# Performance work log

Measured on AMD Instinct MI355X. Metric: run time of the kernel, lower is better.

## Reference

```python
import jax, jax.numpy as jnp
import numpy as np

E = 1024   # embed_dim
H = 16     # num_heads
D = E // H # head_dim
T = 1024   # tgt_len
S = 1024   # src_len
B = 2      # batch
DELTA = 1.0
SCALE = D ** -0.5


def setup_inputs() -> dict:
    key = jax.random.key(0)
    ks = jax.random.split(key, 16)
    def lin(k, o, i):
        return jax.random.normal(k, (o, i), dtype=jnp.float32) / np.float32(np.sqrt(i))
    return {
        'query': jax.random.normal(ks[0], (T, B, E), dtype=jnp.float32),
        'key_in': jax.random.normal(ks[1], (S, B, E), dtype=jnp.float32),
        'value': jax.random.normal(ks[2], (S, B, E), dtype=jnp.float32),
        'Wq': lin(ks[3], E, E), 'bq': jnp.zeros((E,), jnp.float32),
        'Wk': lin(ks[4], E, E), 'bk': jnp.zeros((E,), jnp.float32),
        'Wv': lin(ks[5], E, E), 'bv': jnp.zeros((E,), jnp.float32),
        'Whq': lin(ks[6], E, E), 'bhq': jnp.zeros((E,), jnp.float32),
        'Whk': lin(ks[7], E, E), 'bhk': jnp.zeros((E,), jnp.float32),
        'Wwp': lin(ks[8], E, E), 'bwp': jnp.zeros((E,), jnp.float32),
        'Wvp': lin(ks[9], 1, E), 'bvp': jnp.zeros((1,), jnp.float32),
        'Wo': lin(ks[10], E, E), 'bo': jnp.zeros((E,), jnp.float32),
    }


def _heads(x, L):
    # (L, B, E) -> (B*H, L, D); E splits as (H, D) so flat index is b*H + h
    return x.reshape(L, B * H, D).transpose(1, 0, 2)


def reference(query, key_in, value, Wq, bq, Wk, bk, Wv, bv, Whq, bhq, Whk, bhk,
              Wwp, bwp, Wvp, bvp, Wo, bo):
    q = (query @ Wq.T + bq) * SCALE
    k = key_in @ Wk.T + bk
    v = value @ Wv.T + bv
    hq = query @ Whq.T + bhq
    hk = key_in @ Whk.T + bhk

    qh, hqh = _heads(q, T), _heads(hq, T)
    kh, hkh, vh = _heads(k, S), _heads(hk, S), _heads(v, S)

    # content attention logits  [B*H, T, S]
    attn = jnp.einsum('btd,bsd->bts', qh, kh)

    # Gaussian center: expected source position from hq/hk alignment
    align = jax.nn.softmax(jnp.einsum('btd,bsd->bts', hqh * SCALE, hkh), axis=-1)
    pos = jnp.arange(S, dtype=attn.dtype)          # index_mask
    mean = align @ pos                              # [B*H, T]

    # Gaussian width: per-query scalar via vp(tanh(wp(query)))
    g = (jnp.tanh(query @ Wwp.T + bwp) @ Wvp.T + bvp)[..., 0]   # (T, B)
    sigma = 1.0 + DELTA * jax.nn.sigmoid(g)                      # (T, B)
    sigma_bh = jnp.broadcast_to(sigma[:, :, None], (T, B, H)).reshape(T, B * H).T

    gauss = -((pos[None, None, :] - mean[:, :, None]) ** 2) / (
        2.0 * sigma_bh[:, :, None] ** 2)

    probs = jax.nn.softmax(attn + gauss, axis=-1)
    out = jnp.einsum('bts,bsd->btd', probs, vh)     # [B*H, T, D]
    out = out.transpose(1, 0, 2).reshape(T, B, E)
    return out @ Wo.T + bo
```

## Files before the change

kernel.cpp:

```cpp
#include <hip/hip_runtime.h>
#include <hip/hip_bf16.h>
#include <hip/hip_fp16.h>

#define T_ 1024
#define S_ 1024
#define B_ 2
#define H_ 16
#define D_ 64
#define E_ 1024
#define M_ (T_*B_)
#define SCALE_ 0.125f
#define LOG2E_ 1.4426950408889634f

typedef __attribute__((ext_vector_type(8))) short short8;
typedef __attribute__((ext_vector_type(8))) _Float16 half8;
typedef __attribute__((ext_vector_type(4))) float f32x4;

#define EXP2 __builtin_amdgcn_exp2f

__device__ __forceinline__ ushort f2bf(float x) {
  unsigned u = __float_as_uint(x);
  unsigned r = (u + 0x7fffu + ((u >> 16) & 1u)) >> 16;
  return (ushort)r;
}
__device__ __forceinline__ float bf2f(ushort h) {
  return __uint_as_float(((unsigned)h) << 16);
}
__device__ __forceinline__ ushort f2h(float x) {
  __half h = __float2half(x);
  return *(ushort*)&h;
}
__device__ __forceinline__ void gld16(const void* g, void* l) {
  __builtin_amdgcn_global_load_lds(
      (const __attribute__((address_space(1))) void*)g,
      (__attribute__((address_space(3))) void*)l, 16, 0, 0);
}
__device__ __forceinline__ unsigned cvtpk_bf16(float a, float b) {
  unsigned u;
  asm("v_cvt_pk_bf16_f32 %0, %1, %2" : "=v"(u) : "v"(a), "v"(b));
  return u;
}

#define SWZ(r, col) ((r)*64 + ((col) ^ (((r)&7)<<3)))

struct CvtDesc { const float* src; ushort* bf; ushort* h16; int n4; };
struct CvtArgs { CvtDesc d[10]; };

__global__ __launch_bounds__(256) void cvt_kernel(CvtArgs a) {
  const CvtDesc d = a.d[blockIdx.y];
  const int stride = gridDim.x * 256;
  for (int i = blockIdx.x*256 + threadIdx.x; i < d.n4; i += stride) {
    float4 v = ((const float4*)d.src)[i];
    float vals[4] = {v.x, v.y, v.z, v.w};
    if (d.bf) {
      ushort h[4];
      #pragma unroll
      for (int j = 0; j < 4; ++j) h[j] = f2bf(vals[j]);
      ((ushort4*)d.bf)[i] = make_ushort4(h[0],h[1],h[2],h[3]);
    }
    if (d.h16) {
      ushort h[4];
      #pragma unroll
      for (int j = 0; j < 4; ++j) h[j] = f2h(vals[j]);
      ((ushort4*)d.h16)[i] = make_ushort4(h[0],h[1],h[2],h[3]);
    }
  }
}

struct SegP { const ushort* A; const ushort* W; const float* bias;
              ushort* outb; float* outf; float scale; int flags; };
struct GemmArgs { SegP s[6]; };

__global__ __launch_bounds__(256) void gemm_mfma(GemmArgs args) {
  __shared__ ushort sA[2][128*64];
  __shared__ ushort sW[2][128*64];
  const SegP sg = args.s[blockIdx.x >> 3];
  const int n0 = (blockIdx.x & 7) * 128;
  const int m0 = blockIdx.y * 128;
  const int tid = threadIdx.x, wv = tid >> 6, lane = tid & 63;
  const int c = lane & 15, g = lane >> 4;
  const int wr = wv >> 1, wc = wv & 1;
  const int lrow = lane >> 3;
  const int scol = ((lane & 7) ^ lrow) * 8;

  size_t aoff[4], woff[4];
  #pragma unroll
  for (int j = 0; j < 4; ++j) {
    int rg = wv + j*4;
    aoff[j] = (size_t)(m0 + rg*8 + lrow)*1024 + scol;
    woff[j] = (size_t)(n0 + rg*8 + lrow)*1024 + scol;
  }

  const bool isfp16 = (sg.flags & 2) != 0;
  f32x4 acc[4][4] = {};
  #pragma unroll
  for (int j = 0; j < 4; ++j) {
    int rg = wv + j*4;
    gld16(sg.A + aoff[j], &sA[0][rg*512]);
    gld16(sg.W + woff[j], &sW[0][rg*512]);
  }
  __syncthreads();

  for (int t = 0; t < 16; ++t) {
    const int cur = t & 1;
    if (t < 15) {
      const int k0 = (t+1)*64;
      #pragma unroll
      for (int j = 0; j < 4; ++j) {
        int rg = wv + j*4;
        gld16(sg.A + aoff[j] + k0, &sA[cur^1][rg*512]);
        gld16(sg.W + woff[j] + k0, &sW[cur^1][rg*512]);
      }
    }
    #pragma unroll
    for (int ks = 0; ks < 2; ++ks) {
      short8 af[4], wf[4];
      #pragma unroll
      for (int mi = 0; mi < 4; ++mi)
        af[mi] = *(const short8*)&sA[cur][SWZ(wr*64 + mi*16 + c, ks*32 + g*8)];
      #pragma unroll
      for (int ni = 0; ni < 4; ++ni)
        wf[ni] = *(const short8*)&sW[cur][SWZ(wc*64 + ni*16 + c, ks*32 + g*8)];
      if (isfp16) {
        #pragma unroll
        for (int mi = 0; mi < 4; ++mi)
          #pragma unroll
          for (int ni = 0; ni < 4; ++ni)
            acc[mi][ni] = __builtin_amdgcn_mfma_f32_16x16x32_f16(
                *(half8*)&af[mi], *(half8*)&wf[ni], acc[mi][ni], 0, 0, 0);
      } else {
        #pragma unroll
        for (int mi = 0; mi < 4; ++mi)
          #pragma unroll
          for (int ni = 0; ni < 4; ++ni)
            acc[mi][ni] = __builtin_amdgcn_mfma_f32_16x16x32_bf16(
                af[mi], wf[ni], acc[mi][ni], 0, 0, 0);
      }
    }
    __syncthreads();
  }

  #pragma unroll
  for (int ni = 0; ni < 4; ++ni) {
    int col = n0 + wc*64 + ni*16 + c;
    float bias = sg.bias[col];
    #pragma unroll
    for (int mi = 0; mi < 4; ++mi) {
      #pragma unroll
      for (int r = 0; r < 4; ++r) {
        int row = m0 + wr*64 + mi*16 + 4*g + r;
        float val = (acc[mi][ni][r] + bias) * sg.scale;
        if (sg.flags & 1) val = tanhf(val);
        if (isfp16)       sg.outb[(size_t)row*1024 + col] = f2h(val);
        else if (sg.outf) sg.outf[(size_t)row*1024 + col] = val;
        else              sg.outb[(size_t)row*1024 + col] = f2bf(val);
      }
    }
  }
}

__global__ __launch_bounds__(64) void vp_sigma(const ushort* __restrict__ wp,
    const float* __restrict__ Wvp, const float* __restrict__ bvp,
    float* __restrict__ sigma) {
  const int m = blockIdx.x;
  const int lane = threadIdx.x;
  float acc = 0.f;
  #pragma unroll
  for (int it = 0; it < 2; ++it) {
    int e = lane*8 + it*512;
    short8 a = *(const short8*)&wp[(size_t)m*E_ + e];
    float4 w0 = *(const float4*)&Wvp[e];
    float4 w1 = *(const float4*)&Wvp[e+4];
    acc += bf2f((ushort)a[0])*w0.x + bf2f((ushort)a[1])*w0.y
         + bf2f((ushort)a[2])*w0.z + bf2f((ushort)a[3])*w0.w
         + bf2f((ushort)a[4])*w1.x + bf2f((ushort)a[5])*w1.y
         + bf2f((ushort)a[6])*w1.z + bf2f((ushort)a[7])*w1.w;
  }
  #pragma unroll
  for (int o = 32; o; o >>= 1) acc += __shfl_xor(acc, o);
  if (lane == 0) {
    float gg = acc + bvp[0];
    sigma[m] = 1.f + 1.f/(1.f + __expf(-gg));
  }
}

__global__ __launch_bounds__(256) void attn_mfma(
    const ushort* __restrict__ q_bf, const ushort* __restrict__ k_bf,
    const ushort* __restrict__ v_bf,
    const ushort* __restrict__ hq_h16, const ushort* __restrict__ hk_h16,
    const float* __restrict__ sigma, ushort* __restrict__ ctx) {
  __shared__ ushort sK[2][64*64];
  __shared__ ushort sV[2][64*64];
  __shared__ ushort sP[4*16*64];

  const int bh = blockIdx.y;
  const int b = bh >> 4, h = bh & 15;
  const int t0 = blockIdx.x * 64;
  const int tid = threadIdx.x;
  const int wv = tid >> 6, lane = tid & 63;
  const int c = lane & 15, g = lane >> 4;
  const int qbase = t0 + wv * 16;
  const size_t rowstr = (size_t)B_ * E_;
  const size_t qoff = ((size_t)(qbase + c) * B_ + b) * E_ + h * 64;

  short8 qf[2];
  half8  hqf[2];
  #pragma unroll
  for (int cs = 0; cs < 2; ++cs) {
    qf[cs]  = *(const short8*)&q_bf[qoff + cs*32 + g*8];
    hqf[cs] = *(const half8*)&hq_h16[qoff + cs*32 + g*8];
  }

  const int str0 = wv*16 + (lane >> 3);
  const int str1 = str0 + 8;
  const int chk0 = ((lane & 7) ^ (str0 & 7)) * 8;
  const int chk1 = ((lane & 7) ^ (str1 & 7)) * 8;
  const int ldsst = (wv*16) * 64;

  float den = 0.f, num = 0.f;
  {
    gld16(hk_h16 + ((size_t)str0 * B_ + b) * E_ + h*64 + chk0, &sK[0][ldsst]);
    gld16(hk_h16 + ((size_t)str1 * B_ + b) * E_ + h*64 + chk1, &sK[0][ldsst + 512]);
    __syncthreads();
    for (int t = 0; t < 16; ++t) {
      const ushort* kb = sK[t & 1];
      if (t < 15) {
        int s0n = (t+1) * 64;
        gld16(hk_h16 + ((size_t)(s0n + str0) * B_ + b) * E_ + h*64 + chk0,
              &sK[(t+1) & 1][ldsst]);
        gld16(hk_h16 + ((size_t)(s0n + str1) * B_ + b) * E_ + h*64 + chk1,
              &sK[(t+1) & 1][ldsst + 512]);
      }
      f32x4 acc[4] = {};
      __builtin_amdgcn_s_setprio(1);
      #pragma unroll
      for (int m = 0; m < 4; ++m)
        #pragma unroll
        for (int cs = 0; cs < 2; ++cs)
          acc[m] = __builtin_amdgcn_mfma_f32_16x16x32_f16(
              *(const half8*)&kb[SWZ(c + 16*m, cs*32 + g*8)], hqf[cs], acc[m], 0,0,0);
      __builtin_amdgcn_s_setprio(0);

      float fs = (float)(t*64 + 4*g);
      #pragma unroll
      for (int m = 0; m < 4; ++m)
        #pragma unroll
        for (int r = 0; r < 4; ++r) {
          float e = EXP2(acc[m][r]);
          den += e;
          num += e * (fs + (float)(16*m + r));
        }
      __syncthreads();
    }
  }
  den += __shfl_xor(den, 16); den += __shfl_xor(den, 32);
  num += __shfl_xor(num, 16); num += __shfl_xor(num, 32);
  const float meanq = num / den;
  const float sg = sigma[(size_t)(qbase + c) * B_ + b];
  const float fct = -LOG2E_ / (2.f * sg * sg);

  f32x4 accO[4] = {};
  float denq = 0.f;
  {
    gld16(k_bf + ((size_t)str0 * B_ + b) * E_ + h*64 + chk0, &sK[0][ldsst]);
    gld16(k_bf + ((size_t)str1 * B_ + b) * E_ + h*64 + chk1, &sK[0][ldsst + 512]);
    {
      int s2 = (tid & 31) * 2, d0 = (tid >> 5) * 8;
      size_t off0 = ((size_t)s2 * B_ + b) * E_ + h * 64 + d0;
      uint4 ra = *(const uint4*)&v_bf[off0];
      uint4 rb = *(const uint4*)&v_bf[off0 + rowstr];
      const ushort* pa = (const ushort*)&ra;
      const ushort* pb = (const ushort*)&rb;
      #pragma unroll
      for (int j = 0; j < 8; ++j)
        *(unsigned*)&sV[0][SWZ(d0 + j, s2)] = (unsigned)pa[j] | ((unsigned)pb[j] << 16);
    }
    __syncthreads();

    const int s2v = (tid & 31) * 2, d0v = (tid >> 5) * 8;
    for (int t = 0; t < 16; ++t) {
      const int cur = t & 1;
      const ushort* kb = sK[cur];
      const ushort* vb = sV[cur];
      uint4 ra, rb;
      if (t < 15) {
        int s0n = (t+1) * 64;
        gld16(k_bf + ((size_t)(s0n + str0) * B_ + b) * E_ + h*64 + chk0,
              &sK[cur^1][ldsst]);
        gld16(k_bf + ((size_t)(s0n + str1) * B_ + b) * E_ + h*64 + chk1,
              &sK[cur^1][ldsst + 512]);
        size_t off0 = ((size_t)(s0n + s2v) * B_ + b) * E_ + h * 64 + d0v;
        ra = *(const uint4*)&v_bf[off0];
        rb = *(const uint4*)&v_bf[off0 + rowstr];
      }

      f32x4 accL[4] = {};
      __builtin_amdgcn_s_setprio(1);
      #pragma unroll
      for (int m = 0; m < 4; ++m)
        #pragma unroll
        for (int cs = 0; cs < 2; ++cs)
          accL[m] = __builtin_amdgcn_mfma_f32_16x16x32_bf16(
              *(const short8*)&kb[SWZ(c + 16*m, cs*32 + g*8)], qf[cs], accL[m], 0,0,0);
      __builtin_amdgcn_s_setprio(0);

      float fs = (float)(t*64 + 4*g);
      float psum = 0.f;
      #pragma unroll
      for (int m = 0; m < 4; ++m) {
        float pr[4];
        #pragma unroll
        for (int r = 0; r < 4; ++r) {
          float dd = fs + (float)(16*m + r) - meanq;
          pr[r] = EXP2(accL[m][r] + fct * dd * dd);
          psum += pr[r];
        }
        uint2 uu;
        uu.x = cvtpk_bf16(pr[0], pr[1]);
        uu.y = cvtpk_bf16(pr[2], pr[3]);
        *(uint2*)&sP[wv*1024 + SWZ(c, 16*m + 4*g)] = uu;
      }
      denq += psum;

      __builtin_amdgcn_s_setprio(1);
      #pragma unroll
      for (int n = 0; n < 4; ++n)
        #pragma unroll
        for (int cs = 0; cs < 2; ++cs)
          accO[n] = __builtin_amdgcn_mfma_f32_16x16x32_bf16(
              *(const short8*)&sP[wv*1024 + SWZ(c, cs*32 + 8*g)],
              *(const short8*)&vb[SWZ(c + 16*n, cs*32 + 8*g)],
              accO[n], 0,0,0);
      __builtin_amdgcn_s_setprio(0);

      if (t < 15) {
        const ushort *pa = (const ushort*)&ra, *pb = (const ushort*)&rb;
        #pragma unroll
        for (int j = 0; j < 8; ++j)
          *(unsigned*)&sV[cur^1][SWZ(d0v + j, s2v)] = (unsigned)pa[j] | ((unsigned)pb[j] << 16);
      }
      __syncthreads();
    }
  }

  denq += __shfl_xor(denq, 16);
  denq += __shfl_xor(denq, 32);
  float dinv[4];
  #pragma unroll
  for (int r = 0; r < 4; ++r) dinv[r] = 1.f / __shfl(denq, 4*g + r);

  #pragma unroll
  for (int r = 0; r < 4; ++r) {
    size_t row = ((size_t)(qbase + 4*g + r) * B_ + b) * E_ + h * 64;
    #pragma unroll
    for (int n = 0; n < 4; ++n)
      ctx[row + 16*n + c] = f2bf(accO[n][r] * dinv[r]);
  }
}

extern "C" void kernel_launch(void* const* d_in, const int* in_sizes, int n_in,
                              void* d_out, int out_size, void* d_ws, size_t ws_size,
                              hipStream_t stream) {
  const float* query  = (const float*)d_in[0];
  const float* key_in = (const float*)d_in[1];
  const float* value  = (const float*)d_in[2];
  const float* Wq  = (const float*)d_in[3];  const float* bq  = (const float*)d_in[4];
  const float* Wk  = (const float*)d_in[5];  const float* bk  = (const float*)d_in[6];
  const float* Wv  = (const float*)d_in[7];  const float* bv  = (const float*)d_in[8];
  const float* Whq = (const float*)d_in[9];  const float* bhq = (const float*)d_in[10];
  const float* Whk = (const float*)d_in[11]; const float* bhk = (const float*)d_in[12];
  const float* Wwp = (const float*)d_in[13]; const float* bwp = (const float*)d_in[14];
  const float* Wvp = (const float*)d_in[15]; const float* bvp = (const float*)d_in[16];
  const float* Wo  = (const float*)d_in[17]; const float* bo  = (const float*)d_in[18];

  const size_t AU = (size_t)M_ * E_;
  const size_t WU = (size_t)E_ * E_;
  char* p = (char*)d_ws;
  float*  sig       = (float*)p;  p += 16384;
  ushort* query_bf  = (ushort*)p; p += AU*2;
  ushort* key_bf    = (ushort*)p; p += AU*2;
  ushort* value_bf  = (ushort*)p; p += AU*2;
  ushort* query_h16 = (ushort*)p; p += AU*2;
  ushort* key_h16   = (ushort*)p; p += AU*2;
  ushort* Whq_h16   = (ushort*)p; p += WU*2;
  ushort* Whk_h16   = (ushort*)p; p += WU*2;
  ushort* Wq_bf     = (ushort*)p; p += WU*2;
  ushort* Wk_bf     = (ushort*)p; p += WU*2;
  ushort* Wv_bf     = (ushort*)p; p += WU*2;
  ushort* Wwp_bf    = (ushort*)p; p += WU*2;
  ushort* Wo_bf     = (ushort*)p; p += WU*2;
  ushort* hq_h16    = (ushort*)p; p += AU*2;
  ushort* hk_h16    = (ushort*)p; p += AU*2;
  ushort* q_bf      = (ushort*)p; p += AU*2;
  ushort* k_bf      = (ushort*)p; p += AU*2;
  ushort* v_out     = (ushort*)p; p += AU*2;
  ushort* wp_bf     = (ushort*)p; p += AU*2;
  ushort* ctx_bf    = query_h16;

  {
    CvtArgs a{};
    a.d[0] = {query,  query_bf, query_h16, (int)(AU/4)};
    a.d[1] = {key_in, key_bf,   key_h16,   (int)(AU/4)};
    a.d[2] = {value,  value_bf, nullptr,   (int)(AU/4)};
    a.d[3] = {Whq,    nullptr,  Whq_h16,   (int)(WU/4)};
    a.d[4] = {Whk,    nullptr,  Whk_h16,   (int)(WU/4)};
    a.d[5] = {Wq,     Wq_bf,    nullptr,   (int)(WU/4)};
    a.d[6] = {Wk,     Wk_bf,    nullptr,   (int)(WU/4)};
    a.d[7] = {Wv,     Wv_bf,    nullptr,   (int)(WU/4)};
    a.d[8] = {Wwp,    Wwp_bf,   nullptr,   (int)(WU/4)};
    a.d[9] = {Wo,     Wo_bf,    nullptr,   (int)(WU/4)};
    cvt_kernel<<<dim3(128, 10), 256, 0, stream>>>(a);
  }
  {
    GemmArgs a{};
    a.s[0] = {query_bf,  Wq_bf,   bq,  q_bf,   nullptr, SCALE_*LOG2E_, 0};
    a.s[1] = {query_bf,  Wwp_bf,  bwp, wp_bf,  nullptr, 1.f,           1};
    a.s[2] = {key_bf,    Wk_bf,   bk,  k_bf,   nullptr, 1.f,           0};
    a.s[3] = {value_bf,  Wv_bf,   bv,  v_out,  nullptr, 1.f,           0};
    a.s[4] = {query_h16, Whq_h16, bhq, hq_h16, nullptr, SCALE_*LOG2E_, 2};
    a.s[5] = {key_h16,   Whk_h16, bhk, hk_h16, nullptr, 1.f,           2};
    gemm_mfma<<<dim3(48, 16), 256, 0, stream>>>(a);
  }
  vp_sigma<<<dim3(M_), dim3(64), 0, stream>>>(wp_bf, Wvp, bvp, sig);
  attn_mfma<<<dim3(T_/64, B_*H_), dim3(256), 0, stream>>>(
      q_bf, k_bf, v_out, hq_h16, hk_h16, sig, ctx_bf);
  {
    GemmArgs a{};
    a.s[0] = {ctx_bf, Wo_bf, bo, nullptr, (float*)d_out, 1.f, 0};
    gemm_mfma<<<dim3(8, 16), 256, 0, stream>>>(a);
  }
}
```

Before: 137.4 us.

## Remap blocks to XCDs for L2 locality and single-buffer GEMM LDS

Grids become 1D, and block ids are remapped so that consecutive blocks landing on the same XCD (round-robin dispatch across the eight XCDs) share the same weight columns or the same attention head, which should improve L2 reuse. The GEMM also drops LDS double buffering in favour of a single buffer with load-then-sync per k-step. That halves LDS use and may raise occupancy, but it removes the overlap of global loads with MFMA work. The single-buffer loop appears to rely on the trailing barrier to avoid overwriting data still being read.

```diff
diff --git a/kernel.cpp b/kernel.cpp
--- a/kernel.cpp
+++ b/kernel.cpp
@@ -72,11 +72,15 @@
 struct GemmArgs { SegP s[6]; };
 
 __global__ __launch_bounds__(256) void gemm_mfma(GemmArgs args) {
-  __shared__ ushort sA[2][128*64];
-  __shared__ ushort sW[2][128*64];
-  const SegP sg = args.s[blockIdx.x >> 3];
-  const int n0 = (blockIdx.x & 7) * 128;
-  const int m0 = blockIdx.y * 128;
+  __shared__ ushort sA[128*64];
+  __shared__ ushort sW[128*64];
+  const int id = blockIdx.x;
+  const int xcd = id & 7, loc = id >> 3;
+  const int x = xcd * (gridDim.x >> 7) + (loc >> 4);
+  const int y = loc & 15;
+  const SegP sg = args.s[x >> 3];
+  const int n0 = (x & 7) * 128;
+  const int m0 = y * 128;
   const int tid = threadIdx.x, wv = tid >> 6, lane = tid & 63;
   const int c = lane & 15, g = lane >> 4;
   const int wr = wv >> 1, wc = wv & 1;
@@ -93,34 +97,24 @@
 
   const bool isfp16 = (sg.flags & 2) != 0;
   f32x4 acc[4][4] = {};
-  #pragma unroll
-  for (int j = 0; j < 4; ++j) {
-    int rg = wv + j*4;
-    gld16(sg.A + aoff[j], &sA[0][rg*512]);
-    gld16(sg.W + woff[j], &sW[0][rg*512]);
-  }
-  __syncthreads();
-
   for (int t = 0; t < 16; ++t) {
-    const int cur = t & 1;
-    if (t < 15) {
-      const int k0 = (t+1)*64;
-      #pragma unroll
-      for (int j = 0; j < 4; ++j) {
-        int rg = wv + j*4;
-        gld16(sg.A + aoff[j] + k0, &sA[cur^1][rg*512]);
-        gld16(sg.W + woff[j] + k0, &sW[cur^1][rg*512]);
-      }
-    }
+    const int k0 = t*64;
+    #pragma unroll
+    for (int j = 0; j < 4; ++j) {
+      int rg = wv + j*4;
+      gld16(sg.A + aoff[j] + k0, &sA[rg*512]);
+      gld16(sg.W + woff[j] + k0, &sW[rg*512]);
+    }
+    __syncthreads();
     #pragma unroll
     for (int ks = 0; ks < 2; ++ks) {
       short8 af[4], wf[4];
       #pragma unroll
       for (int mi = 0; mi < 4; ++mi)
-        af[mi] = *(const short8*)&sA[cur][SWZ(wr*64 + mi*16 + c, ks*32 + g*8)];
+        af[mi] = *(const short8*)&sA[SWZ(wr*64 + mi*16 + c, ks*32 + g*8)];
       #pragma unroll
       for (int ni = 0; ni < 4; ++ni)
-        wf[ni] = *(const short8*)&sW[cur][SWZ(wc*64 + ni*16 + c, ks*32 + g*8)];
+        wf[ni] = *(const short8*)&sW[SWZ(wc*64 + ni*16 + c, ks*32 + g*8)];
       if (isfp16) {
         #pragma unroll
         for (int mi = 0; mi < 4; ++mi)
@@ -193,9 +187,11 @@
   __shared__ ushort sV[2][64*64];
   __shared__ ushort sP[4*16*64];
 
-  const int bh = blockIdx.y;
+  const int id = blockIdx.x;
+  const int loc = id >> 3;
+  const int bh = (id & 7) * 4 + (loc >> 4);
   const int b = bh >> 4, h = bh & 15;
-  const int t0 = blockIdx.x * 64;
+  const int t0 = (loc & 15) * 64;
   const int tid = threadIdx.x;
   const int wv = tid >> 6, lane = tid & 63;
   const int c = lane & 15, g = lane >> 4;
@@ -419,14 +415,14 @@
     a.s[3] = {value_bf,  Wv_bf,   bv,  v_out,  nullptr, 1.f,           0};
     a.s[4] = {query_h16, Whq_h16, bhq, hq_h16, nullptr, SCALE_*LOG2E_, 2};
     a.s[5] = {key_h16,   Whk_h16, bhk, hk_h16, nullptr, 1.f,           2};
-    gemm_mfma<<<dim3(48, 16), 256, 0, stream>>>(a);
+    gemm_mfma<<<dim3(768), 256, 0, stream>>>(a);
   }
   vp_sigma<<<dim3(M_), dim3(64), 0, stream>>>(wp_bf, Wvp, bvp, sig);
-  attn_mfma<<<dim3(T_/64, B_*H_), dim3(256), 0, stream>>>(
+  attn_mfma<<<dim3(512), 256, 0, stream>>>(
       q_bf, k_bf, v_out, hq_h16, hk_h16, sig, ctx_bf);
   {
     GemmArgs a{};
     a.s[0] = {ctx_bf, Wo_bf, bo, nullptr, (float*)d_out, 1.f, 0};
-    gemm_mfma<<<dim3(8, 16), 256, 0, stream>>>(a);
-  }
-}
+    gemm_mfma<<<dim3(128), 256, 0, stream>>>(a);
+  }
+}
```

After: 132.9 us. -3.3%, faster.
